# Optimization experiments

Measured on AMD Instinct MI355X. Metric: run time of the kernel, lower is better.

Reference implementation:

```python
import jax, jax.numpy as jnp
import numpy as np

M = 1024      # num_inducing
B = 131072    # batch of query points (original module is per-query; we vmap/vectorize)
EPS_D = 1e-8
JITTER = 1e-4

Z_SCALE = np.array([0.15, 0.1, 0.05, 800.0, 20.0], dtype=np.float32)
Z_SHIFT = np.array([0.0, 0.0, 0.0, 600.0, 5.0], dtype=np.float32)


def setup_inputs() -> dict:
    key = jax.random.key(0)
    k1, k2 = jax.random.split(key)
    x_star = jax.random.normal(k1, (B, 5), dtype=jnp.float32)
    # learnable params, sized/initialized per the flax module
    log_lengthscale = jnp.log(jnp.array([0.2, 0.15, 0.1, 400.0, 15.0], dtype=jnp.float32))
    log_variance = jnp.asarray(jnp.log(0.08), dtype=jnp.float32)
    Z_raw = jax.random.uniform(k2, (M, 5), dtype=jnp.float32)  # uniform(scale=1.0) init
    return {"x_star": x_star, "log_lengthscale": log_lengthscale,
            "log_variance": log_variance, "Z_raw": Z_raw}


def _pairwise_sqdist(A, Bm):
    # ||a-b||^2 via gemm; A:(n,d), Bm:(m,d) -> (n,m)
    aa = jnp.sum(A * A, axis=-1)
    bb = jnp.sum(Bm * Bm, axis=-1)
    d2 = aa[:, None] + bb[None, :] - 2.0 * (A @ Bm.T)
    return jnp.maximum(d2, 0.0)


def _matern52(d2, prior_var):
    d = jnp.sqrt(d2 + EPS_D)
    s = jnp.sqrt(5.0) * d
    return prior_var * (1.0 + s + (5.0 / 3.0) * (d * d)) * jnp.exp(-s)


def reference(x_star, log_lengthscale, log_variance, Z_raw):
    ls = jnp.exp(log_lengthscale)                # (5,)
    prior_var = jnp.exp(log_variance)            # scalar
    Z = Z_raw * jnp.asarray(Z_SCALE) + jnp.asarray(Z_SHIFT)  # (M,5)
    inv_ls = 1.0 / (ls + 1e-8)
    Zs = Z * inv_ls                              # lengthscale-scaled inducing pts
    Xs = x_star * inv_ls                         # (B,5)

    K_ZZ = _matern52(_pairwise_sqdist(Zs, Zs), prior_var)            # (M,M)
    K_ZZ_inv = jnp.linalg.inv(K_ZZ + JITTER * jnp.eye(M, dtype=K_ZZ.dtype))

    k_xZ = _matern52(_pairwise_sqdist(Xs, Zs), prior_var)            # (B,M)
    red = jnp.sum(k_xZ * (k_xZ @ K_ZZ_inv), axis=-1)                 # (B,)
    variance = jnp.maximum(prior_var - red, 1e-6)
    return jnp.sqrt(variance)                                        # (B,) predictive std
```

## Files before the change

kernel.cpp:

```cpp
#include <hip/hip_runtime.h>
#include <math.h>

#define B_TOT 131072
#define M_N   1024
#define BS    128
#define NBK   8

typedef float    f32x4 __attribute__((ext_vector_type(4)));
typedef _Float16 f16x8 __attribute__((ext_vector_type(8)));

enum : size_t {
    OFF_KF  = 0,
    OFF_LF  = (size_t)4 << 20,
    OFF_WF  = (size_t)8 << 20,
    OFF_WPH = (size_t)12 << 20,
    OFF_WPL = (size_t)14 << 20,
    OFF_PF  = (size_t)16 << 20,
    OFF_ZT  = ((size_t)16 << 20) + 256,
};

__device__ __constant__ float c_zscale[5] = {0.15f, 0.1f, 0.05f, 800.0f, 20.0f};
__device__ __constant__ float c_zshift[5] = {0.0f, 0.0f, 0.0f, 600.0f, 5.0f};

__global__ __launch_bounds__(256) void k_build(const float* __restrict__ log_ls,
                                               const float* __restrict__ log_var,
                                               const float* __restrict__ Zraw,
                                               float* __restrict__ Kf,
                                               float* __restrict__ pf,
                                               float* __restrict__ Zst) {
    __shared__ float ps[6];
    __shared__ float zsi[5];
    int tid = threadIdx.x;
    if (tid < 5) ps[tid] = 1.0f / (__expf(log_ls[tid]) + 1e-8f);
    if (tid == 5) ps[5] = __expf(log_var[0]);
    __syncthreads();
    int i = blockIdx.x >> 2;
    int j = (blockIdx.x & 3) * 256 + tid;
    if (tid < 5) zsi[tid] = (Zraw[i * 5 + tid] * c_zscale[tid] + c_zshift[tid]) * ps[tid];
    __syncthreads();
    float d2 = 0.0f;
#pragma unroll
    for (int d = 0; d < 5; ++d) {
        float zj = (Zraw[j * 5 + d] * c_zscale[d] + c_zshift[d]) * ps[d];
        float df = zsi[d] - zj;
        d2 += df * df;
    }
    float dd = d2 + 1e-8f;
    float dist = sqrtf(dd);
    float s = 2.23606798f * dist;
    float v = ps[5] * (1.0f + s + 1.66666667f * dd) * __expf(-s);
    if (i == j) v += 1e-4f;
    Kf[(size_t)i * M_N + j] = v;
    if (blockIdx.x < 4) {
        int m = blockIdx.x * 256 + tid;
#pragma unroll
        for (int d = 0; d < 5; ++d)
            Zst[d * M_N + m] = (Zraw[m * 5 + d] * c_zscale[d] + c_zshift[d]) * ps[d];
    }
    if (blockIdx.x == 4 && tid < 6) pf[tid] = ps[tid];
}

__global__ __launch_bounds__(512) void kw_diag(float* __restrict__ Kf,
                                               float* __restrict__ Wf, int kb) {
    __shared__ float As[128][129];
    __shared__ float sinv[128];
    int tid = threadIdx.x;
    int r0 = kb * BS;
    for (int idx = tid; idx < BS * BS; idx += 512) {
        int rr = idx >> 7, cc = idx & 127;
        As[rr][cc] = Kf[(size_t)(r0 + rr) * M_N + r0 + cc];
    }
    __syncthreads();

    int r = tid & 127, q = tid >> 7;
    for (int p = 0; p < 16; ++p) {
        int j0 = p * 8;
        for (int j = j0; j < j0 + 8; ++j) {
            if (tid == j) {
                float d = sqrtf(As[j][j]);
                As[j][j] = d;
                sinv[j] = 1.0f / d;
            }
            __syncthreads();
            float arj = 0.0f;
            if (q == 0 && r > j) {
                arj = As[r][j] * sinv[j];
                As[r][j] = arj;
            }
            __syncthreads();
            if (q == 0 && r > j) {
#pragma unroll
                for (int c = j + 1; c < j0 + 8; ++c)
                    As[r][c] -= arj * As[c][j];
            }
        }
        __syncthreads();
        if (p < 15) {
            float a[8];
#pragma unroll
            for (int t = 0; t < 8; ++t) a[t] = As[r][j0 + t];
            for (int c = j0 + 8 + q; c < 128; c += 4) {
                if (r >= c) {
                    float s = As[r][c];
#pragma unroll
                    for (int t = 0; t < 8; ++t) s -= a[t] * As[c][j0 + t];
                    As[r][c] = s;
                }
            }
        }
        __syncthreads();
    }

    if (tid < 128) {
        int c = tid;
        for (int rb = 0; rb < 16; ++rb) {
            int r0b = rb * 8;
            if (c >= r0b + 8) continue;
            float s[8];
#pragma unroll
            for (int i = 0; i < 8; ++i) s[i] = 0.0f;
            for (int t = 0; t < r0b; ++t) {
                if (t >= c) {
                    float xt = (t == c) ? sinv[c] : As[c][t];
#pragma unroll
                    for (int i = 0; i < 8; ++i) s[i] += As[r0b + i][t] * xt;
                }
            }
            float xloc[8];
#pragma unroll
            for (int i = 0; i < 8; ++i) {
                int rr = r0b + i;
                float v = 0.0f;
                if (rr >= c) {
                    v = ((rr == c) ? 1.0f : 0.0f) - s[i];
#pragma unroll
                    for (int t2 = 0; t2 < i; ++t2) {
                        int tt = r0b + t2;
                        if (tt >= c) v -= As[rr][tt] * xloc[t2];
                    }
                    v *= sinv[rr];
                    if (rr > c) As[c][rr] = v;
                }
                xloc[i] = v;
            }
        }
    }
    __syncthreads();
    for (int idx = tid; idx < BS * BS; idx += 512) {
        int rr = idx >> 7, cc = idx & 127;
        if (rr >= cc)
            Wf[(size_t)(r0 + rr) * M_N + r0 + cc] = (rr == cc) ? sinv[rr] : As[cc][rr];
    }
}

static __device__ void d_strip(const float* __restrict__ Kf, const float* __restrict__ Wf,
                               int cb, int row0, float (*S)[129],
                               float (*Ast)[17], float (*Wst)[128], int tid) {
    int c = tid & 127, q = tid >> 7;
    float acc[32];
#pragma unroll
    for (int i = 0; i < 32; ++i) acc[i] = 0.0f;
    for (int tc = 0; tc < 8; ++tc) {
        int tb = tc * 16;
        __syncthreads();
        for (int idx = tid; idx < 64 * 16; idx += 256) {
            int rr = idx >> 4, tt = idx & 15;
            Ast[rr][tt] = Kf[(size_t)(row0 + rr) * M_N + cb + tb + tt];
        }
        for (int idx = tid; idx < 128 * 16; idx += 256) {
            int cc = idx >> 4, tt = idx & 15;
            Wst[tt][cc] = (tb + tt <= cc) ? Wf[(size_t)(cb + cc) * M_N + cb + tb + tt] : 0.0f;
        }
        __syncthreads();
#pragma unroll
        for (int t = 0; t < 16; ++t) {
            float w = Wst[t][c];
#pragma unroll
            for (int i = 0; i < 32; ++i) acc[i] += Ast[q * 32 + i][t] * w;
        }
    }
    __syncthreads();
#pragma unroll
    for (int i = 0; i < 32; ++i) S[q * 32 + i][c] = acc[i];
}

static __device__ void d_diag256(float (*As)[129], float* sinv,
                                 float* __restrict__ Wf, int r0, int tid) {
    int r = tid & 127, half = tid >> 7;
    for (int p = 0; p < 16; ++p) {
        int j0 = p * 8;
        for (int j = j0; j < j0 + 8; ++j) {
            if (tid == j) {
                float d = sqrtf(As[j][j]);
                As[j][j] = d;
                sinv[j] = 1.0f / d;
            }
            __syncthreads();
            float arj = 0.0f;
            if (half == 0 && r > j) {
                arj = As[r][j] * sinv[j];
                As[r][j] = arj;
            }
            __syncthreads();
            if (half == 0 && r > j) {
#pragma unroll
                for (int c = j + 1; c < j0 + 8; ++c)
                    As[r][c] -= arj * As[c][j];
            }
        }
        __syncthreads();
        if (p < 15) {
            float a[8];
#pragma unroll
            for (int t = 0; t < 8; ++t) a[t] = As[r][j0 + t];
            for (int c = j0 + 8 + half; c < 128; c += 2) {
                if (r >= c) {
                    float s = As[r][c];
#pragma unroll
                    for (int t = 0; t < 8; ++t) s -= a[t] * As[c][j0 + t];
                    As[r][c] = s;
                }
            }
        }
        __syncthreads();
    }
    if (tid < 128) {
        int c = tid;
        for (int rb = 0; rb < 16; ++rb) {
            int r0b = rb * 8;
            if (c >= r0b + 8) continue;
            float s[8];
#pragma unroll
            for (int i = 0; i < 8; ++i) s[i] = 0.0f;
            for (int t = 0; t < r0b; ++t) {
                if (t >= c) {
                    float xt = (t == c) ? sinv[c] : As[c][t];
#pragma unroll
                    for (int i = 0; i < 8; ++i) s[i] += As[r0b + i][t] * xt;
                }
            }
            float xloc[8];
#pragma unroll
            for (int i = 0; i < 8; ++i) {
                int rr = r0b + i;
                float v = 0.0f;
                if (rr >= c) {
                    v = ((rr == c) ? 1.0f : 0.0f) - s[i];
#pragma unroll
                    for (int t2 = 0; t2 < i; ++t2) {
                        int tt = r0b + t2;
                        if (tt >= c) v -= As[rr][tt] * xloc[t2];
                    }
                    v *= sinv[rr];
                    if (rr > c) As[c][rr] = v;
                }
                xloc[i] = v;
            }
        }
    }
    __syncthreads();
    for (int idx = tid; idx < BS * BS; idx += 256) {
        int rr = idx >> 7, cc = idx & 127;
        if (rr >= cc)
            Wf[(size_t)(r0 + rr) * M_N + r0 + cc] = (rr == cc) ? sinv[rr] : As[cc][rr];
    }
}

__global__ __launch_bounds__(256) void kw_step(float* __restrict__ Kf,
                                               float* __restrict__ Wf,
                                               float* __restrict__ Lf, int kb) {
    __shared__ float SA[64][129];
    __shared__ float SB[64][129];
    __shared__ float Ast[64][17];
    __shared__ float Wst[16][128];
    __shared__ float As[128][129];
    __shared__ float sinv[128];
    int tid = threadIdx.x;
    int base = (kb + 1) * BS;
    int cb = kb * BS;
    int tx = tid & 15, ty = tid >> 4;

    if (blockIdx.x == 0) {
        d_strip(Kf, Wf, cb, base, SA, Ast, Wst, tid);
        d_strip(Kf, Wf, cb, base + 64, SB, Ast, Wst, tid);
        __syncthreads();
#pragma unroll
        for (int qq = 0; qq < 3; ++qq) {
            int qy = (qq == 0) ? 0 : 1;
            int qx = (qq == 2) ? 1 : 0;
            float (*Sy)[129] = qy ? SB : SA;
            float (*Sx)[129] = qx ? SB : SA;
            float acc[4][4];
#pragma unroll
            for (int i = 0; i < 4; ++i)
#pragma unroll
                for (int j = 0; j < 4; ++j) acc[i][j] = 0.0f;
            for (int t = 0; t < 128; ++t) {
                float a[4], b[4];
#pragma unroll
                for (int i = 0; i < 4; ++i) a[i] = Sy[ty * 4 + i][t];
#pragma unroll
                for (int j = 0; j < 4; ++j) b[j] = Sx[tx * 4 + j][t];
#pragma unroll
                for (int i = 0; i < 4; ++i)
#pragma unroll
                    for (int j = 0; j < 4; ++j) acc[i][j] = fmaf(a[i], b[j], acc[i][j]);
            }
#pragma unroll
            for (int i = 0; i < 4; ++i)
#pragma unroll
                for (int j = 0; j < 4; ++j)
                    As[qy * 64 + ty * 4 + i][qx * 64 + tx * 4 + j] =
                        Kf[(size_t)(base + qy * 64 + ty * 4 + i) * M_N +
                           base + qx * 64 + tx * 4 + j] - acc[i][j];
        }
        for (int idx = tid; idx < 64 * 128; idx += 256) {
            int rr = idx >> 7, cc = idx & 127;
            Lf[(size_t)(base + rr) * M_N + cb + cc]      = SA[rr][cc];
            Lf[(size_t)(base + 64 + rr) * M_N + cb + cc] = SB[rr][cc];
        }
        __syncthreads();
        d_diag256(As, sinv, Wf, base, tid);
    } else {
        int vp = blockIdx.x + 2;
        int by = 0;
        while ((by + 1) * (by + 2) / 2 <= vp) ++by;
        int bx = vp - by * (by + 1) / 2;
        int gr0 = base + by * 64, gc0 = base + bx * 64;
        d_strip(Kf, Wf, cb, gr0, SA, Ast, Wst, tid);
        if (bx != by) d_strip(Kf, Wf, cb, gc0, SB, Ast, Wst, tid);
        float (*PB)[129] = (bx == by) ? SA : SB;
        __syncthreads();
        float acc[4][4];
#pragma unroll
        for (int i = 0; i < 4; ++i)
#pragma unroll
            for (int j = 0; j < 4; ++j) acc[i][j] = 0.0f;
        for (int t = 0; t < 128; ++t) {
            float a[4], b[4];
#pragma unroll
            for (int i = 0; i < 4; ++i) a[i] = SA[ty * 4 + i][t];
#pragma unroll
            for (int j = 0; j < 4; ++j) b[j] = PB[tx * 4 + j][t];
#pragma unroll
            for (int i = 0; i < 4; ++i)
#pragma unroll
                for (int j = 0; j < 4; ++j) acc[i][j] = fmaf(a[i], b[j], acc[i][j]);
        }
#pragma unroll
        for (int i = 0; i < 4; ++i)
#pragma unroll
            for (int j = 0; j < 4; ++j)
                Kf[(size_t)(gr0 + ty * 4 + i) * M_N + gc0 + tx * 4 + j] -= acc[i][j];
        if (by == bx) {
            for (int idx = tid; idx < 64 * 128; idx += 256)
                Lf[(size_t)(gr0 + (idx >> 7)) * M_N + cb + (idx & 127)] =
                    SA[idx >> 7][idx & 127];
        }
    }
}

__global__ __launch_bounds__(512) void kw_trtri(const float* __restrict__ Lf,
                                                float* __restrict__ Wf) {
    __shared__ float Ls[128][33];
    __shared__ float Ws[32][33];
    __shared__ float Whist[6][128][33];
    __shared__ float Ps[128][33];
    int j  = blockIdx.y;
    int ct = blockIdx.x;
    int c0 = j * BS + ct * 32;
    int tid = threadIdx.x;
    int rq = tid >> 2, cq = tid & 3;

    for (int i = j + 1; i < 8; ++i) {
        float acc[8];
#pragma unroll
        for (int c = 0; c < 8; ++c) acc[c] = 0.0f;
        for (int t = j; t < i; ++t) {
            for (int ch = 0; ch < 4; ++ch) {
                int tb = t * BS + ch * 32;
                __syncthreads();
                for (int idx = tid; idx < 128 * 32; idx += 512) {
                    int rr = idx >> 5, tt = idx & 31;
                    Ls[rr][tt] = Lf[(size_t)(i * BS + rr) * M_N + tb + tt];
                }
                if (t == j) {
                    for (int idx = tid; idx < 32 * 32; idx += 512) {
                        int tt = idx >> 5, cc = idx & 31;
                        int gr = tb + tt, gc = c0 + cc;
                        Ws[tt][cc] = (gr >= gc) ? Wf[(size_t)gr * M_N + gc] : 0.0f;
                    }
                }
                __syncthreads();
                if (t == j) {
#pragma unroll
                    for (int tt = 0; tt < 32; ++tt) {
                        float l = Ls[rq][tt];
#pragma unroll
                        for (int c = 0; c < 8; ++c)
                            acc[c] = fmaf(l, Ws[tt][cq * 8 + c], acc[c]);
                    }
                } else {
                    const float (*Wh)[33] = Whist[t - j - 1];
#pragma unroll
                    for (int tt = 0; tt < 32; ++tt) {
                        float l = Ls[rq][tt];
#pragma unroll
                        for (int c = 0; c < 8; ++c)
                            acc[c] = fmaf(l, Wh[ch * 32 + tt][cq * 8 + c], acc[c]);
                    }
                }
            }
        }
        __syncthreads();
#pragma unroll
        for (int c = 0; c < 8; ++c) Ps[rq][cq * 8 + c] = acc[c];
        float a2[8];
#pragma unroll
        for (int c = 0; c < 8; ++c) a2[c] = 0.0f;
        for (int ch = 0; ch < 4; ++ch) {
            __syncthreads();
            for (int idx = tid; idx < 128 * 32; idx += 512) {
                int rr = idx >> 5, tt = idx & 31;
                Ls[rr][tt] = (rr >= ch * 32 + tt)
                           ? Wf[(size_t)(i * BS + rr) * M_N + i * BS + ch * 32 + tt] : 0.0f;
            }
            __syncthreads();
#pragma unroll
            for (int tt = 0; tt < 32; ++tt) {
                float l = Ls[rq][tt];
#pragma unroll
                for (int c = 0; c < 8; ++c)
                    a2[c] = fmaf(l, Ps[ch * 32 + tt][cq * 8 + c], a2[c]);
            }
        }
        __syncthreads();
#pragma unroll
        for (int c = 0; c < 8; ++c) {
            float v = -a2[c];
            Wf[(size_t)(i * BS + rq) * M_N + c0 + cq * 8 + c] = v;
            if (i < 7) Whist[i - j - 1][rq][cq * 8 + c] = v;
        }
        __syncthreads();
    }
}

__global__ void kw_pack(const float* __restrict__ Wf, _Float16* __restrict__ Wph,
                        _Float16* __restrict__ Wpl) {
    int T = blockIdx.x * 256 + threadIdx.x;
    int lane = T & 63, fid = T >> 6;
    int jn = fid & 63, kik = fid >> 6;
    int ki = kik & 3, kc = kik >> 2;
    int j  = jn * 16 + (lane & 15);
    int kb = kc * 128 + ki * 32 + (lane >> 4) * 8;
    f16x8 h, lo;
#pragma unroll
    for (int e = 0; e < 8; ++e) {
        int k = kb + e;
        float v = (k <= j) ? Wf[(size_t)j * M_N + k] : 0.0f;
        _Float16 hh = (_Float16)v;
        h[e]  = hh;
        lo[e] = (_Float16)(v - (float)hh);
    }
    size_t off = (size_t)fid * 512 + lane * 8;
    *(f16x8*)(Wph + off) = h;
    *(f16x8*)(Wpl + off) = lo;
}

__global__ __launch_bounds__(512, 1) void k_mm(const float* __restrict__ x_star,
                                               const float* __restrict__ pf,
                                               const float* __restrict__ Zst,
                                               const _Float16* __restrict__ Wph,
                                               const _Float16* __restrict__ Wpl,
                                               float* __restrict__ out, int Bq) {
    __shared__ __align__(16) char kls[2][64 * 256];
    __shared__ float red_l[64];
    int tid  = threadIdx.x;
    int slab = blockIdx.x;
    int w = tid >> 6, lane = tid & 63;
    int lrow = lane & 15, kgrp = lane >> 4;

    int scc = tid & 15, srow0 = tid >> 4;
    int q0 = slab * 64 + srow0;
    int q1 = q0 + 32;
    int qa = (q0 < Bq) ? q0 : (Bq - 1);
    int qb = (q1 < Bq) ? q1 : (Bq - 1);
    float xa0 = x_star[(size_t)qa * 5 + 0] * pf[0];
    float xa1 = x_star[(size_t)qa * 5 + 1] * pf[1];
    float xa2 = x_star[(size_t)qa * 5 + 2] * pf[2];
    float xa3 = x_star[(size_t)qa * 5 + 3] * pf[3];
    float xa4 = x_star[(size_t)qa * 5 + 4] * pf[4];
    float xb0 = x_star[(size_t)qb * 5 + 0] * pf[0];
    float xb1 = x_star[(size_t)qb * 5 + 1] * pf[1];
    float xb2 = x_star[(size_t)qb * 5 + 2] * pf[2];
    float xb3 = x_star[(size_t)qb * 5 + 3] * pf[3];
    float xb4 = x_star[(size_t)qb * 5 + 4] * pf[4];
    float pv = pf[5];
    if (tid < 64) red_l[tid] = 0.0f;

    f32x4 acc[4][8];
#pragma unroll
    for (int mi = 0; mi < 4; ++mi)
#pragma unroll
        for (int nj = 0; nj < 8; ++nj) acc[mi][nj] = (f32x4)(0.0f);

    int jmax_w = (56 + ((w + 7) & 7)) * 16 + 15;
    int swz = (scc * 16) ^ ((srow0 & 15) << 4);
    int soff0 = srow0 * 256 + swz;
    int soff1 = (srow0 + 32) * 256 + swz;

    auto stage = [&](int kc, char* buf) {
        f16x8 h0, h1;
#pragma unroll
        for (int bb = 0; bb < 2; ++bb) {
            int lb = kc * 128 + scc * 8 + bb * 4;
            float z0[4], z1[4], z2[4], z3[4], z4[4];
            *(float4*)z0 = *(const float4*)&Zst[lb];
            *(float4*)z1 = *(const float4*)&Zst[M_N + lb];
            *(float4*)z2 = *(const float4*)&Zst[2 * M_N + lb];
            *(float4*)z3 = *(const float4*)&Zst[3 * M_N + lb];
            *(float4*)z4 = *(const float4*)&Zst[4 * M_N + lb];
#pragma unroll
            for (int e = 0; e < 4; ++e) {
                float dx0 = xa0 - z0[e], dx1 = xa1 - z1[e], dx2 = xa2 - z2[e],
                      dx3 = xa3 - z3[e], dx4 = xa4 - z4[e];
                float d2 = dx0 * dx0 + dx1 * dx1 + dx2 * dx2 + dx3 * dx3 + dx4 * dx4;
                float ddv = d2 + 1e-8f;
                float dist = sqrtf(ddv);
                float sv = 2.23606798f * dist;
                h0[bb * 4 + e] = (_Float16)(pv * (1.0f + sv + 1.66666667f * ddv) * __expf(-sv));
                float ex0 = xb0 - z0[e], ex1 = xb1 - z1[e], ex2 = xb2 - z2[e],
                      ex3 = xb3 - z3[e], ex4 = xb4 - z4[e];
                float e2 = ex0 * ex0 + ex1 * ex1 + ex2 * ex2 + ex3 * ex3 + ex4 * ex4;
                float eev = e2 + 1e-8f;
                float edist = sqrtf(eev);
                float esv = 2.23606798f * edist;
                h1[bb * 4 + e] = (_Float16)(pv * (1.0f + esv + 1.66666667f * eev) * __expf(-esv));
            }
        }
        *(f16x8*)(&buf[soff0]) = h0;
        *(f16x8*)(&buf[soff1]) = h1;
    };

    stage(0, kls[0]);
    __syncthreads();

    for (int kc = 0; kc < 8; ++kc) {
        if (kc < 7) stage(kc + 1, kls[(kc + 1) & 1]);
        const char* cur = kls[kc & 1];
        for (int ki = 0; ki < 4; ++ki) {
            int kmin = kc * 128 + ki * 32;
            if (kmin > jmax_w) break;
            f16x8 A_[4];
#pragma unroll
            for (int mi = 0; mi < 4; ++mi) {
                int row = mi * 16 + lrow;
                int cb  = ki * 64 + kgrp * 16;
                A_[mi] = *(const f16x8*)(&cur[row * 256 + (cb ^ ((row & 15) << 4))]);
            }
#pragma unroll
            for (int nj = 0; nj < 8; ++nj) {
                int jng = nj * 8 + ((w + nj) & 7);
                if (kmin > jng * 16 + 15) continue;
                size_t fo = ((size_t)((kc * 4 + ki) * 64 + jng)) * 512 + lane * 8;
                f16x8 Bh = *(const f16x8*)(Wph + fo);
                f16x8 Bl = *(const f16x8*)(Wpl + fo);
#pragma unroll
                for (int mi = 0; mi < 4; ++mi) {
                    acc[mi][nj] = __builtin_amdgcn_mfma_f32_16x16x32_f16(A_[mi], Bh, acc[mi][nj], 0, 0, 0);
                    acc[mi][nj] = __builtin_amdgcn_mfma_f32_16x16x32_f16(A_[mi], Bl, acc[mi][nj], 0, 0, 0);
                }
            }
        }
        __syncthreads();
    }

#pragma unroll
    for (int mi = 0; mi < 4; ++mi) {
#pragma unroll
        for (int q = 0; q < 4; ++q) {
            float s = 0.0f;
#pragma unroll
            for (int nj = 0; nj < 8; ++nj) s = fmaf(acc[mi][nj][q], acc[mi][nj][q], s);
            s += __shfl_xor(s, 1);
            s += __shfl_xor(s, 2);
            s += __shfl_xor(s, 4);
            s += __shfl_xor(s, 8);
            if (lrow == 0) atomicAdd(&red_l[mi * 16 + kgrp * 4 + q], s);
        }
    }
    __syncthreads();
    if (tid < 64) {
        int b = slab * 64 + tid;
        if (b < Bq) out[b] = sqrtf(fmaxf(pv - red_l[tid], 1e-6f));
    }
}

extern "C" void kernel_launch(void* const* d_in, const int* in_sizes, int n_in,
                              void* d_out, int out_size, void* d_ws, size_t ws_size,
                              hipStream_t stream) {
    const float* x_star  = (const float*)d_in[0];
    const float* log_ls  = (const float*)d_in[1];
    const float* log_var = (const float*)d_in[2];
    const float* Z_raw   = (const float*)d_in[3];
    float* out = (float*)d_out;
    int Bq = in_sizes[0] / 5;

    char* ws = (char*)d_ws;
    float*     Kf  = (float*)(ws + OFF_KF);
    float*     Lf  = (float*)(ws + OFF_LF);
    float*     Wf  = (float*)(ws + OFF_WF);
    _Float16*  Wph = (_Float16*)(ws + OFF_WPH);
    _Float16*  Wpl = (_Float16*)(ws + OFF_WPL);
    float*     pf  = (float*)(ws + OFF_PF);
    float*     Zst = (float*)(ws + OFF_ZT);

    k_build<<<4096, 256, 0, stream>>>(log_ls, log_var, Z_raw, Kf, pf, Zst);
    kw_diag<<<1, 512, 0, stream>>>(Kf, Wf, 0);

    for (int kb = 0; kb < NBK - 1; ++kb) {
        int nt = (NBK - 1 - kb) * 2;
        int grid = nt * (nt + 1) / 2 - 2;
        kw_step<<<grid, 256, 0, stream>>>(Kf, Wf, Lf, kb);
    }

    kw_trtri<<<dim3(4, 7), 512, 0, stream>>>(Lf, Wf);
    kw_pack<<<512, 256, 0, stream>>>(Wf, Wph, Wpl);

    int slabs = (Bq + 63) / 64;
    k_mm<<<slabs, 512, 0, stream>>>(x_star, pf, Zst, Wph, Wpl, out, Bq);
}
```

Measured before the change: 3.680 ms.

## Precompute kernel matrix to workspace and split triangular GEMM across column halves

After: 3.591 ms. 2.4% less time.

```diff
diff --git a/kernel.cpp b/kernel.cpp
--- a/kernel.cpp
+++ b/kernel.cpp
@@ -17,6 +17,8 @@
     OFF_WPL = (size_t)14 << 20,
     OFF_PF  = (size_t)16 << 20,
     OFF_ZT  = ((size_t)16 << 20) + 256,
+    OFF_RED = (size_t)17 << 20,
+    OFF_AP  = (size_t)32 << 20,
 };
 
 __device__ __constant__ float c_zscale[5] = {0.15f, 0.1f, 0.05f, 800.0f, 20.0f};
@@ -60,8 +62,51 @@
     if (blockIdx.x == 4 && tid < 6) pf[tid] = ps[tid];
 }
 
+__global__ __launch_bounds__(256) void k_gen(const float* __restrict__ x_star,
+                                             const float* __restrict__ pf,
+                                             const float* __restrict__ Zst,
+                                             _Float16* __restrict__ Ap, int Bq) {
+    int tid = threadIdx.x;
+    int lane = tid & 63;
+    int fid = blockIdx.x * 4 + (tid >> 6);
+    int mi = fid & 3, kk = (fid >> 2) & 31, slab = fid >> 7;
+    int row = slab * 64 + mi * 16 + (lane & 15);
+    int k0 = kk * 32 + (lane >> 4) * 8;
+    int rc = (row < Bq) ? row : (Bq - 1);
+    float x0 = x_star[(size_t)rc * 5 + 0] * pf[0];
+    float x1 = x_star[(size_t)rc * 5 + 1] * pf[1];
+    float x2 = x_star[(size_t)rc * 5 + 2] * pf[2];
+    float x3 = x_star[(size_t)rc * 5 + 3] * pf[3];
+    float x4 = x_star[(size_t)rc * 5 + 4] * pf[4];
+    float pv = pf[5];
+    float z0[8], z1[8], z2[8], z3[8], z4[8];
+    *(float4*)&z0[0] = *(const float4*)&Zst[k0];
+    *(float4*)&z0[4] = *(const float4*)&Zst[k0 + 4];
+    *(float4*)&z1[0] = *(const float4*)&Zst[M_N + k0];
+    *(float4*)&z1[4] = *(const float4*)&Zst[M_N + k0 + 4];
+    *(float4*)&z2[0] = *(const float4*)&Zst[2 * M_N + k0];
+    *(float4*)&z2[4] = *(const float4*)&Zst[2 * M_N + k0 + 4];
+    *(float4*)&z3[0] = *(const float4*)&Zst[3 * M_N + k0];
+    *(float4*)&z3[4] = *(const float4*)&Zst[3 * M_N + k0 + 4];
+    *(float4*)&z4[0] = *(const float4*)&Zst[4 * M_N + k0];
+    *(float4*)&z4[4] = *(const float4*)&Zst[4 * M_N + k0 + 4];
+    f16x8 h;
+#pragma unroll
+    for (int e = 0; e < 8; ++e) {
+        float dx0 = x0 - z0[e], dx1 = x1 - z1[e], dx2 = x2 - z2[e],
+              dx3 = x3 - z3[e], dx4 = x4 - z4[e];
+        float d2 = dx0 * dx0 + dx1 * dx1 + dx2 * dx2 + dx3 * dx3 + dx4 * dx4;
+        float dd = d2 + 1e-8f;
+        float dist = sqrtf(dd);
+        float sv = 2.23606798f * dist;
+        h[e] = (_Float16)(pv * (1.0f + sv + 1.66666667f * dd) * __expf(-sv));
+    }
+    *(f16x8*)(&Ap[(size_t)fid * 512 + lane * 8]) = h;
+}
+
 __global__ __launch_bounds__(512) void kw_diag(float* __restrict__ Kf,
                                                float* __restrict__ Wf, int kb) {
+    if (blockIdx.x) return;
     __shared__ float As[128][129];
     __shared__ float sinv[128];
     int tid = threadIdx.x;
@@ -279,6 +324,8 @@
     int base = (kb + 1) * BS;
     int cb = kb * BS;
     int tx = tid & 15, ty = tid >> 4;
+    int nt = (NBK - 1 - kb) * 2;
+    int ntile = nt * (nt + 1) / 2;
 
     if (blockIdx.x == 0) {
         d_strip(Kf, Wf, cb, base, SA, Ast, Wst, tid);
@@ -323,6 +370,7 @@
         d_diag256(As, sinv, Wf, base, tid);
     } else {
         int vp = blockIdx.x + 2;
+        if (vp >= ntile) return;
         int by = 0;
         while ((by + 1) * (by + 2) / 2 <= vp) ++by;
         int bx = vp - by * (by + 1) / 2;
@@ -467,96 +515,146 @@
     *(f16x8*)(Wpl + off) = lo;
 }
 
-__global__ __launch_bounds__(512, 1) void k_mm(const float* __restrict__ x_star,
-                                               const float* __restrict__ pf,
-                                               const float* __restrict__ Zst,
-                                               const _Float16* __restrict__ Wph,
-                                               const _Float16* __restrict__ Wpl,
-                                               float* __restrict__ out, int Bq) {
-    __shared__ __align__(16) char kls[2][64 * 256];
+__global__ __launch_bounds__(512) void k_mm(const _Float16* __restrict__ Ap,
+                                            const _Float16* __restrict__ Wph,
+                                            const _Float16* __restrict__ Wpl,
+                                            float* __restrict__ redp, int Bq) {
     __shared__ float red_l[64];
+    int tid  = threadIdx.x;
+    int slab = blockIdx.x, pp = blockIdx.y;
+    int w = tid >> 6, lane = tid & 63;
+    int lrow = lane & 15, kgrp = lane >> 4;
+    if (tid < 64) red_l[tid] = 0.0f;
+    __syncthreads();
+
+    f32x4 acc[4][4];
+#pragma unroll
+    for (int mi = 0; mi < 4; ++mi)
+#pragma unroll
+        for (int nj = 0; nj < 4; ++nj) acc[mi][nj] = (f32x4)(0.0f);
+
+    int jmax_w = (pp * 32 + 24 + ((w + 3) & 7)) * 16 + 15;
+    const _Float16* Abase = Ap + (size_t)slab * 128 * 512 + lane * 8;
+    const _Float16* Whb = Wph + lane * 8;
+    const _Float16* Wlb = Wpl + lane * 8;
+
+    for (int kt = 0; kt < 32; ++kt) {
+        int kmin = kt * 32;
+        if (kmin > jmax_w) break;
+        f16x8 A_[4];
+#pragma unroll
+        for (int mi = 0; mi < 4; ++mi)
+            A_[mi] = *(const f16x8*)(Abase + (size_t)(kt * 4 + mi) * 512);
+#pragma unroll
+        for (int nj = 0; nj < 4; ++nj) {
+            int jng = pp * 32 + nj * 8 + ((w + nj) & 7);
+            if (kmin > jng * 16 + 15) continue;
+            size_t fo = (size_t)(kt * 64 + jng) * 512;
+            f16x8 Bh = *(const f16x8*)(Whb + fo);
+            f16x8 Bl = *(const f16x8*)(Wlb + fo);
+#pragma unroll
+            for (int mi = 0; mi < 4; ++mi) {
+                acc[mi][nj] = __builtin_amdgcn_mfma_f32_16x16x32_f16(A_[mi], Bh, acc[mi][nj], 0, 0, 0);
+                acc[mi][nj] = __builtin_amdgcn_mfma_f32_16x16x32_f16(A_[mi], Bl, acc[mi][nj], 0, 0, 0);
+            }
+        }
+    }
+
+#pragma unroll
+    for (int mi = 0; mi < 4; ++mi) {
+#pragma unroll
+        for (int q = 0; q < 4; ++q) {
+            float s = 0.0f;
+#pragma unroll
+            for (int nj = 0; nj < 4; ++nj) s = fmaf(acc[mi][nj][q], acc[mi][nj][q], s);
+            s += __shfl_xor(s, 1);
+            s += __shfl_xor(s, 2);
+            s += __shfl_xor(s, 4);
+            s += __shfl_xor(s, 8);
+            if (lrow == 0) atomicAdd(&red_l[mi * 16 + kgrp * 4 + q], s);
+        }
+    }
+    __syncthreads();
+    if (tid < 64) {
+        int b = slab * 64 + tid;
+        if (b < Bq) redp[(size_t)pp * Bq + b] = red_l[tid];
+    }
+}
+
+__global__ void k_fin(const float* __restrict__ redp, const float* __restrict__ pf,
+                      float* __restrict__ out, int Bq) {
+    int b = blockIdx.x * 256 + threadIdx.x;
+    if (b < Bq) {
+        float red = redp[b] + redp[(size_t)Bq + b];
+        out[b] = sqrtf(fmaxf(pf[5] - red, 1e-6f));
+    }
+}
+
+__global__ __launch_bounds__(512, 1) void k_mm_fused(const float* __restrict__ x_star,
+                                                     const float* __restrict__ pf,
+                                                     const float* __restrict__ Zst,
+                                                     const _Float16* __restrict__ Wph,
+                                                     const _Float16* __restrict__ Wpl,
+                                                     float* __restrict__ out, int Bq) {
+    __shared__ __align__(16) char kls[32 * 256];
+    __shared__ float red_l[32];
     int tid  = threadIdx.x;
     int slab = blockIdx.x;
     int w = tid >> 6, lane = tid & 63;
     int lrow = lane & 15, kgrp = lane >> 4;
-
-    int scc = tid & 15, srow0 = tid >> 4;
-    int q0 = slab * 64 + srow0;
-    int q1 = q0 + 32;
-    int qa = (q0 < Bq) ? q0 : (Bq - 1);
-    int qb = (q1 < Bq) ? q1 : (Bq - 1);
-    float xa0 = x_star[(size_t)qa * 5 + 0] * pf[0];
-    float xa1 = x_star[(size_t)qa * 5 + 1] * pf[1];
-    float xa2 = x_star[(size_t)qa * 5 + 2] * pf[2];
-    float xa3 = x_star[(size_t)qa * 5 + 3] * pf[3];
-    float xa4 = x_star[(size_t)qa * 5 + 4] * pf[4];
-    float xb0 = x_star[(size_t)qb * 5 + 0] * pf[0];
-    float xb1 = x_star[(size_t)qb * 5 + 1] * pf[1];
-    float xb2 = x_star[(size_t)qb * 5 + 2] * pf[2];
-    float xb3 = x_star[(size_t)qb * 5 + 3] * pf[3];
-    float xb4 = x_star[(size_t)qb * 5 + 4] * pf[4];
+    int srow = tid >> 4, scc = tid & 15;
+    int qrow = slab * 32 + srow;
+    int qc = (qrow < Bq) ? qrow : (Bq - 1);
+    float xv0 = x_star[(size_t)qc * 5 + 0] * pf[0];
+    float xv1 = x_star[(size_t)qc * 5 + 1] * pf[1];
+    float xv2 = x_star[(size_t)qc * 5 + 2] * pf[2];
+    float xv3 = x_star[(size_t)qc * 5 + 3] * pf[3];
+    float xv4 = x_star[(size_t)qc * 5 + 4] * pf[4];
     float pv = pf[5];
-    if (tid < 64) red_l[tid] = 0.0f;
-
-    f32x4 acc[4][8];
-#pragma unroll
-    for (int mi = 0; mi < 4; ++mi)
+    if (tid < 32) red_l[tid] = 0.0f;
+
+    f32x4 acc[2][8];
+#pragma unroll
+    for (int mi = 0; mi < 2; ++mi)
 #pragma unroll
         for (int nj = 0; nj < 8; ++nj) acc[mi][nj] = (f32x4)(0.0f);
-
     int jmax_w = (56 + ((w + 7) & 7)) * 16 + 15;
-    int swz = (scc * 16) ^ ((srow0 & 15) << 4);
-    int soff0 = srow0 * 256 + swz;
-    int soff1 = (srow0 + 32) * 256 + swz;
-
-    auto stage = [&](int kc, char* buf) {
-        f16x8 h0, h1;
+    int soff = srow * 256 + ((scc * 16) ^ ((srow & 15) << 4));
+
+    for (int kc = 0; kc < 8; ++kc) {
+        int lb = kc * 128 + scc * 8;
+        f16x8 hv;
 #pragma unroll
         for (int bb = 0; bb < 2; ++bb) {
-            int lb = kc * 128 + scc * 8 + bb * 4;
             float z0[4], z1[4], z2[4], z3[4], z4[4];
-            *(float4*)z0 = *(const float4*)&Zst[lb];
-            *(float4*)z1 = *(const float4*)&Zst[M_N + lb];
-            *(float4*)z2 = *(const float4*)&Zst[2 * M_N + lb];
-            *(float4*)z3 = *(const float4*)&Zst[3 * M_N + lb];
-            *(float4*)z4 = *(const float4*)&Zst[4 * M_N + lb];
+            *(float4*)z0 = *(const float4*)&Zst[lb + 4 * bb];
+            *(float4*)z1 = *(const float4*)&Zst[M_N + lb + 4 * bb];
+            *(float4*)z2 = *(const float4*)&Zst[2 * M_N + lb + 4 * bb];
+            *(float4*)z3 = *(const float4*)&Zst[3 * M_N + lb + 4 * bb];
+            *(float4*)z4 = *(const float4*)&Zst[4 * M_N + lb + 4 * bb];
 #pragma unroll
             for (int e = 0; e < 4; ++e) {
-                float dx0 = xa0 - z0[e], dx1 = xa1 - z1[e], dx2 = xa2 - z2[e],
-                      dx3 = xa3 - z3[e], dx4 = xa4 - z4[e];
+                float dx0 = xv0 - z0[e], dx1 = xv1 - z1[e], dx2 = xv2 - z2[e],
+                      dx3 = xv3 - z3[e], dx4 = xv4 - z4[e];
                 float d2 = dx0 * dx0 + dx1 * dx1 + dx2 * dx2 + dx3 * dx3 + dx4 * dx4;
-                float ddv = d2 + 1e-8f;
-                float dist = sqrtf(ddv);
+                float dd = d2 + 1e-8f;
+                float dist = sqrtf(dd);
                 float sv = 2.23606798f * dist;
-                h0[bb * 4 + e] = (_Float16)(pv * (1.0f + sv + 1.66666667f * ddv) * __expf(-sv));
-                float ex0 = xb0 - z0[e], ex1 = xb1 - z1[e], ex2 = xb2 - z2[e],
-                      ex3 = xb3 - z3[e], ex4 = xb4 - z4[e];
-                float e2 = ex0 * ex0 + ex1 * ex1 + ex2 * ex2 + ex3 * ex3 + ex4 * ex4;
-                float eev = e2 + 1e-8f;
-                float edist = sqrtf(eev);
-                float esv = 2.23606798f * edist;
-                h1[bb * 4 + e] = (_Float16)(pv * (1.0f + esv + 1.66666667f * eev) * __expf(-esv));
-            }
-        }
-        *(f16x8*)(&buf[soff0]) = h0;
-        *(f16x8*)(&buf[soff1]) = h1;
-    };
-
-    stage(0, kls[0]);
-    __syncthreads();
-
-    for (int kc = 0; kc < 8; ++kc) {
-        if (kc < 7) stage(kc + 1, kls[(kc + 1) & 1]);
-        const char* cur = kls[kc & 1];
+                hv[bb * 4 + e] = (_Float16)(pv * (1.0f + sv + 1.66666667f * dd) * __expf(-sv));
+            }
+        }
+        __syncthreads();
+        *(f16x8*)(&kls[soff]) = hv;
+        __syncthreads();
         for (int ki = 0; ki < 4; ++ki) {
             int kmin = kc * 128 + ki * 32;
             if (kmin > jmax_w) break;
-            f16x8 A_[4];
-#pragma unroll
-            for (int mi = 0; mi < 4; ++mi) {
+            f16x8 A_[2];
+#pragma unroll
+            for (int mi = 0; mi < 2; ++mi) {
                 int row = mi * 16 + lrow;
                 int cb  = ki * 64 + kgrp * 16;
-                A_[mi] = *(const f16x8*)(&cur[row * 256 + (cb ^ ((row & 15) << 4))]);
+                A_[mi] = *(const f16x8*)(&kls[row * 256 + (cb ^ ((row & 15) << 4))]);
             }
 #pragma unroll
             for (int nj = 0; nj < 8; ++nj) {
@@ -566,17 +664,15 @@
                 f16x8 Bh = *(const f16x8*)(Wph + fo);
                 f16x8 Bl = *(const f16x8*)(Wpl + fo);
 #pragma unroll
-                for (int mi = 0; mi < 4; ++mi) {
+                for (int mi = 0; mi < 2; ++mi) {
                     acc[mi][nj] = __builtin_amdgcn_mfma_f32_16x16x32_f16(A_[mi], Bh, acc[mi][nj], 0, 0, 0);
                     acc[mi][nj] = __builtin_amdgcn_mfma_f32_16x16x32_f16(A_[mi], Bl, acc[mi][nj], 0, 0, 0);
                 }
             }
         }
-        __syncthreads();
-    }
-
-#pragma unroll
-    for (int mi = 0; mi < 4; ++mi) {
+    }
+#pragma unroll
+    for (int mi = 0; mi < 2; ++mi) {
 #pragma unroll
         for (int q = 0; q < 4; ++q) {
             float s = 0.0f;
@@ -590,8 +686,8 @@
         }
     }
     __syncthreads();
-    if (tid < 64) {
-        int b = slab * 64 + tid;
+    if (tid < 32) {
+        int b = slab * 32 + tid;
         if (b < Bq) out[b] = sqrtf(fmaxf(pv - red_l[tid], 1e-6f));
     }
 }
@@ -607,26 +703,38 @@
     int Bq = in_sizes[0] / 5;
 
     char* ws = (char*)d_ws;
-    float*     Kf  = (float*)(ws + OFF_KF);
-    float*     Lf  = (float*)(ws + OFF_LF);
-    float*     Wf  = (float*)(ws + OFF_WF);
-    _Float16*  Wph = (_Float16*)(ws + OFF_WPH);
-    _Float16*  Wpl = (_Float16*)(ws + OFF_WPL);
-    float*     pf  = (float*)(ws + OFF_PF);
-    float*     Zst = (float*)(ws + OFF_ZT);
+    float*     Kf   = (float*)(ws + OFF_KF);
+    float*     Lf   = (float*)(ws + OFF_LF);
+    float*     Wf   = (float*)(ws + OFF_WF);
+    _Float16*  Wph  = (_Float16*)(ws + OFF_WPH);
+    _Float16*  Wpl  = (_Float16*)(ws + OFF_WPL);
+    float*     pf   = (float*)(ws + OFF_PF);
+    float*     Zst  = (float*)(ws + OFF_ZT);
+    float*     redp = (float*)(ws + OFF_RED);
+    _Float16*  Ap   = (_Float16*)(ws + OFF_AP);
+
+    int slabs = (Bq + 63) / 64;
+    size_t ap_bytes = (size_t)slabs * 128 * 512 * 2;
+    bool use_ap = ws_size >= OFF_AP + ap_bytes;
 
     k_build<<<4096, 256, 0, stream>>>(log_ls, log_var, Z_raw, Kf, pf, Zst);
-    kw_diag<<<1, 512, 0, stream>>>(Kf, Wf, 0);
-
+    if (use_ap)
+        k_gen<<<slabs * 32, 256, 0, stream>>>(x_star, pf, Zst, Ap, Bq);
+
+    kw_diag<<<64, 512, 0, stream>>>(Kf, Wf, 0);
     for (int kb = 0; kb < NBK - 1; ++kb) {
         int nt = (NBK - 1 - kb) * 2;
         int grid = nt * (nt + 1) / 2 - 2;
+        if (grid < 64) grid = 64;
         kw_step<<<grid, 256, 0, stream>>>(Kf, Wf, Lf, kb);
     }
-
     kw_trtri<<<dim3(4, 7), 512, 0, stream>>>(Lf, Wf);
     kw_pack<<<512, 256, 0, stream>>>(Wf, Wph, Wpl);
 
-    int slabs = (Bq + 63) / 64;
-    k_mm<<<slabs, 512, 0, stream>>>(x_star, pf, Zst, Wph, Wpl, out, Bq);
-}
+    if (use_ap) {
+        k_mm<<<dim3(slabs, 2), 512, 0, stream>>>(Ap, Wph, Wpl, redp, Bq);
+        k_fin<<<(Bq + 255) / 256, 256, 0, stream>>>(redp, pf, out, Bq);
+    } else {
+        k_mm_fused<<<(Bq + 31) / 32, 512, 0, stream>>>(x_star, pf, Zst, Wph, Wpl, out, Bq);
+    }
+}
```

## Split k_mm output columns into two passes to allow two blocks per CU

Applied to the files above, without the earlier changes.

After: 3.510 ms. -4.6%, faster.

```diff
diff --git a/kernel.cpp b/kernel.cpp
--- a/kernel.cpp
+++ b/kernel.cpp
@@ -62,6 +62,7 @@
 
 __global__ __launch_bounds__(512) void kw_diag(float* __restrict__ Kf,
                                                float* __restrict__ Wf, int kb) {
+    if (blockIdx.x) return;
     __shared__ float As[128][129];
     __shared__ float sinv[128];
     int tid = threadIdx.x;
@@ -279,6 +280,8 @@
     int base = (kb + 1) * BS;
     int cb = kb * BS;
     int tx = tid & 15, ty = tid >> 4;
+    int nt = (NBK - 1 - kb) * 2;
+    int ntile = nt * (nt + 1) / 2;
 
     if (blockIdx.x == 0) {
         d_strip(Kf, Wf, cb, base, SA, Ast, Wst, tid);
@@ -323,6 +326,7 @@
         d_diag256(As, sinv, Wf, base, tid);
     } else {
         int vp = blockIdx.x + 2;
+        if (vp >= ntile) return;
         int by = 0;
         while ((by + 1) * (by + 2) / 2 <= vp) ++by;
         int bx = vp - by * (by + 1) / 2;
@@ -467,13 +471,13 @@
     *(f16x8*)(Wpl + off) = lo;
 }
 
-__global__ __launch_bounds__(512, 1) void k_mm(const float* __restrict__ x_star,
+__global__ __launch_bounds__(512, 2) void k_mm(const float* __restrict__ x_star,
                                                const float* __restrict__ pf,
                                                const float* __restrict__ Zst,
                                                const _Float16* __restrict__ Wph,
                                                const _Float16* __restrict__ Wpl,
                                                float* __restrict__ out, int Bq) {
-    __shared__ __align__(16) char kls[2][64 * 256];
+    __shared__ __align__(16) char kls[64 * 256];
     __shared__ float red_l[64];
     int tid  = threadIdx.x;
     int slab = blockIdx.x;
@@ -498,98 +502,97 @@
     float pv = pf[5];
     if (tid < 64) red_l[tid] = 0.0f;
 
-    f32x4 acc[4][8];
-#pragma unroll
-    for (int mi = 0; mi < 4; ++mi)
-#pragma unroll
-        for (int nj = 0; nj < 8; ++nj) acc[mi][nj] = (f32x4)(0.0f);
-
-    int jmax_w = (56 + ((w + 7) & 7)) * 16 + 15;
     int swz = (scc * 16) ^ ((srow0 & 15) << 4);
     int soff0 = srow0 * 256 + swz;
     int soff1 = (srow0 + 32) * 256 + swz;
 
-    auto stage = [&](int kc, char* buf) {
-        f16x8 h0, h1;
-#pragma unroll
-        for (int bb = 0; bb < 2; ++bb) {
-            int lb = kc * 128 + scc * 8 + bb * 4;
-            float z0[4], z1[4], z2[4], z3[4], z4[4];
-            *(float4*)z0 = *(const float4*)&Zst[lb];
-            *(float4*)z1 = *(const float4*)&Zst[M_N + lb];
-            *(float4*)z2 = *(const float4*)&Zst[2 * M_N + lb];
-            *(float4*)z3 = *(const float4*)&Zst[3 * M_N + lb];
-            *(float4*)z4 = *(const float4*)&Zst[4 * M_N + lb];
-#pragma unroll
-            for (int e = 0; e < 4; ++e) {
-                float dx0 = xa0 - z0[e], dx1 = xa1 - z1[e], dx2 = xa2 - z2[e],
-                      dx3 = xa3 - z3[e], dx4 = xa4 - z4[e];
-                float d2 = dx0 * dx0 + dx1 * dx1 + dx2 * dx2 + dx3 * dx3 + dx4 * dx4;
-                float ddv = d2 + 1e-8f;
-                float dist = sqrtf(ddv);
-                float sv = 2.23606798f * dist;
-                h0[bb * 4 + e] = (_Float16)(pv * (1.0f + sv + 1.66666667f * ddv) * __expf(-sv));
-                float ex0 = xb0 - z0[e], ex1 = xb1 - z1[e], ex2 = xb2 - z2[e],
-                      ex3 = xb3 - z3[e], ex4 = xb4 - z4[e];
-                float e2 = ex0 * ex0 + ex1 * ex1 + ex2 * ex2 + ex3 * ex3 + ex4 * ex4;
-                float eev = e2 + 1e-8f;
-                float edist = sqrtf(eev);
-                float esv = 2.23606798f * edist;
-                h1[bb * 4 + e] = (_Float16)(pv * (1.0f + esv + 1.66666667f * eev) * __expf(-esv));
-            }
-        }
-        *(f16x8*)(&buf[soff0]) = h0;
-        *(f16x8*)(&buf[soff1]) = h1;
-    };
-
-    stage(0, kls[0]);
-    __syncthreads();
-
-    for (int kc = 0; kc < 8; ++kc) {
-        if (kc < 7) stage(kc + 1, kls[(kc + 1) & 1]);
-        const char* cur = kls[kc & 1];
-        for (int ki = 0; ki < 4; ++ki) {
-            int kmin = kc * 128 + ki * 32;
-            if (kmin > jmax_w) break;
-            f16x8 A_[4];
-#pragma unroll
-            for (int mi = 0; mi < 4; ++mi) {
-                int row = mi * 16 + lrow;
-                int cb  = ki * 64 + kgrp * 16;
-                A_[mi] = *(const f16x8*)(&cur[row * 256 + (cb ^ ((row & 15) << 4))]);
-            }
-#pragma unroll
-            for (int nj = 0; nj < 8; ++nj) {
-                int jng = nj * 8 + ((w + nj) & 7);
-                if (kmin > jng * 16 + 15) continue;
-                size_t fo = ((size_t)((kc * 4 + ki) * 64 + jng)) * 512 + lane * 8;
-                f16x8 Bh = *(const f16x8*)(Wph + fo);
-                f16x8 Bl = *(const f16x8*)(Wpl + fo);
+    for (int pp = 0; pp < 2; ++pp) {
+        f32x4 acc[4][4];
+#pragma unroll
+        for (int mi = 0; mi < 4; ++mi)
+#pragma unroll
+            for (int nj = 0; nj < 4; ++nj) acc[mi][nj] = (f32x4)(0.0f);
+
+        int jmax_w = (pp * 32 + 24 + ((w + 3) & 7)) * 16 + 15;
+        int KC = pp ? 8 : 4;
+
+        for (int kc = 0; kc < KC; ++kc) {
+            f16x8 h0, h1;
+#pragma unroll
+            for (int bb = 0; bb < 2; ++bb) {
+                int lb = kc * 128 + scc * 8 + bb * 4;
+                float z0[4], z1[4], z2[4], z3[4], z4[4];
+                *(float4*)z0 = *(const float4*)&Zst[lb];
+                *(float4*)z1 = *(const float4*)&Zst[M_N + lb];
+                *(float4*)z2 = *(const float4*)&Zst[2 * M_N + lb];
+                *(float4*)z3 = *(const float4*)&Zst[3 * M_N + lb];
+                *(float4*)z4 = *(const float4*)&Zst[4 * M_N + lb];
+#pragma unroll
+                for (int e = 0; e < 4; ++e) {
+                    float dx0 = xa0 - z0[e], dx1 = xa1 - z1[e], dx2 = xa2 - z2[e],
+                          dx3 = xa3 - z3[e], dx4 = xa4 - z4[e];
+                    float d2 = dx0 * dx0 + dx1 * dx1 + dx2 * dx2 + dx3 * dx3 + dx4 * dx4;
+                    float dd = d2 + 1e-8f;
+                    float dist = sqrtf(dd);
+                    float sv = 2.23606798f * dist;
+                    h0[bb * 4 + e] = (_Float16)(pv * (1.0f + sv + 1.66666667f * dd) * __expf(-sv));
+                    float ex0 = xb0 - z0[e], ex1 = xb1 - z1[e], ex2 = xb2 - z2[e],
+                          ex3 = xb3 - z3[e], ex4 = xb4 - z4[e];
+                    float e2 = ex0 * ex0 + ex1 * ex1 + ex2 * ex2 + ex3 * ex3 + ex4 * ex4;
+                    float ee = e2 + 1e-8f;
+                    float edist = sqrtf(ee);
+                    float esv = 2.23606798f * edist;
+                    h1[bb * 4 + e] = (_Float16)(pv * (1.0f + esv + 1.66666667f * ee) * __expf(-esv));
+                }
+            }
+            __syncthreads();
+            *(f16x8*)(&kls[soff0]) = h0;
+            *(f16x8*)(&kls[soff1]) = h1;
+            __syncthreads();
+
+            for (int ki = 0; ki < 4; ++ki) {
+                int kmin = kc * 128 + ki * 32;
+                if (kmin > jmax_w) break;
+                f16x8 A_[4];
 #pragma unroll
                 for (int mi = 0; mi < 4; ++mi) {
-                    acc[mi][nj] = __builtin_amdgcn_mfma_f32_16x16x32_f16(A_[mi], Bh, acc[mi][nj], 0, 0, 0);
-                    acc[mi][nj] = __builtin_amdgcn_mfma_f32_16x16x32_f16(A_[mi], Bl, acc[mi][nj], 0, 0, 0);
-                }
-            }
-        }
-        __syncthreads();
-    }
-
-#pragma unroll
-    for (int mi = 0; mi < 4; ++mi) {
-#pragma unroll
-        for (int q = 0; q < 4; ++q) {
-            float s = 0.0f;
-#pragma unroll
-            for (int nj = 0; nj < 8; ++nj) s = fmaf(acc[mi][nj][q], acc[mi][nj][q], s);
-            s += __shfl_xor(s, 1);
-            s += __shfl_xor(s, 2);
-            s += __shfl_xor(s, 4);
-            s += __shfl_xor(s, 8);
-            if (lrow == 0) atomicAdd(&red_l[mi * 16 + kgrp * 4 + q], s);
-        }
-    }
-    __syncthreads();
+                    int row = mi * 16 + lrow;
+                    int cb  = ki * 64 + kgrp * 16;
+                    A_[mi] = *(const f16x8*)(&kls[row * 256 + (cb ^ ((row & 15) << 4))]);
+                }
+#pragma unroll
+                for (int nj = 0; nj < 4; ++nj) {
+                    int jng = pp * 32 + nj * 8 + ((w + nj) & 7);
+                    if (kmin > jng * 16 + 15) continue;
+                    size_t fo = ((size_t)((kc * 4 + ki) * 64 + jng)) * 512 + lane * 8;
+                    f16x8 Bh = *(const f16x8*)(Wph + fo);
+                    f16x8 Bl = *(const f16x8*)(Wpl + fo);
+#pragma unroll
+                    for (int mi = 0; mi < 4; ++mi) {
+                        acc[mi][nj] = __builtin_amdgcn_mfma_f32_16x16x32_f16(A_[mi], Bh, acc[mi][nj], 0, 0, 0);
+                        acc[mi][nj] = __builtin_amdgcn_mfma_f32_16x16x32_f16(A_[mi], Bl, acc[mi][nj], 0, 0, 0);
+                    }
+                }
+            }
+        }
+
+#pragma unroll
+        for (int mi = 0; mi < 4; ++mi) {
+#pragma unroll
+            for (int q = 0; q < 4; ++q) {
+                float s = 0.0f;
+#pragma unroll
+                for (int nj = 0; nj < 4; ++nj) s = fmaf(acc[mi][nj][q], acc[mi][nj][q], s);
+                s += __shfl_xor(s, 1);
+                s += __shfl_xor(s, 2);
+                s += __shfl_xor(s, 4);
+                s += __shfl_xor(s, 8);
+                if (lrow == 0) atomicAdd(&red_l[mi * 16 + kgrp * 4 + q], s);
+            }
+        }
+        __syncthreads();
+    }
+
     if (tid < 64) {
         int b = slab * 64 + tid;
         if (b < Bq) out[b] = sqrtf(fmaxf(pv - red_l[tid], 1e-6f));
@@ -616,14 +619,13 @@
     float*     Zst = (float*)(ws + OFF_ZT);
 
     k_build<<<4096, 256, 0, stream>>>(log_ls, log_var, Z_raw, Kf, pf, Zst);
-    kw_diag<<<1, 512, 0, stream>>>(Kf, Wf, 0);
-
+    kw_diag<<<64, 512, 0, stream>>>(Kf, Wf, 0);
     for (int kb = 0; kb < NBK - 1; ++kb) {
         int nt = (NBK - 1 - kb) * 2;
         int grid = nt * (nt + 1) / 2 - 2;
+        if (grid < 64) grid = 64;
         kw_step<<<grid, 256, 0, stream>>>(Kf, Wf, Lf, kb);
     }
-
     kw_trtri<<<dim3(4, 7), 512, 0, stream>>>(Lf, Wf);
     kw_pack<<<512, 256, 0, stream>>>(Wf, Wph, Wpl);
 
```
